# Optimization experiments

Measured on AMD Instinct MI355X. Metric: run time of the kernel, lower is better.

## Reference

```python
import jax, jax.numpy as jnp
import numpy as np

BATCH = 8192
EMBED_DIM = 256
INPUT_DIM = 3 * EMBED_DIM  # 768
NUM_LAYERS = 4
VOCAB_SIZES = [100000, 100000, 1000]
EPS = 1e-5


def setup_inputs() -> dict:
    key = jax.random.key(0)
    ks = jax.random.split(key, 20)
    inp = {}
    inp["x_p"] = jax.random.randint(ks[0], (BATCH,), 0, VOCAB_SIZES[0])
    inp["x_a"] = jax.random.randint(ks[1], (BATCH,), 0, VOCAB_SIZES[1])
    inp["x_c"] = jax.random.randint(ks[2], (BATCH,), 0, VOCAB_SIZES[2])
    inp["y_true"] = jax.random.uniform(ks[3], (BATCH, 1), dtype=jnp.float32)
    # embedding tables (nn.Embedding default init N(0,1))
    inp["E0"] = jax.random.normal(ks[4], (VOCAB_SIZES[0], EMBED_DIM), dtype=jnp.float32)
    inp["E1"] = jax.random.normal(ks[5], (VOCAB_SIZES[1], EMBED_DIM), dtype=jnp.float32)
    inp["E2"] = jax.random.normal(ks[6], (VOCAB_SIZES[2], EMBED_DIM), dtype=jnp.float32)
    lim = 1.0 / np.sqrt(INPUT_DIM)
    inp["Wd"] = jax.random.uniform(ks[7], (NUM_LAYERS, INPUT_DIM, INPUT_DIM), jnp.float32, -lim, lim)
    inp["bd"] = jnp.zeros((NUM_LAYERS, INPUT_DIM), jnp.float32)
    inp["Ws"] = jax.random.uniform(ks[8], (NUM_LAYERS, INPUT_DIM, INPUT_DIM), jnp.float32, -lim, lim)
    inp["bs"] = jnp.zeros((NUM_LAYERS, INPUT_DIM), jnp.float32)
    inp["wfd"] = jax.random.uniform(ks[9], (INPUT_DIM,), jnp.float32, -lim, lim)
    inp["bfd"] = jax.random.uniform(ks[10], (), jnp.float32, -lim, lim)
    inp["wfs"] = jax.random.uniform(ks[11], (INPUT_DIM,), jnp.float32, -lim, lim)
    inp["bfs"] = jax.random.uniform(ks[12], (), jnp.float32, -lim, lim)
    return inp


def _cross_network(x, W, b, net_id, mask_key):
    # per layer: cross = x @ W[l].T + b[l]; mask = bernoulli(sigmoid(layernorm over FULL tensor)); x += cross*mask
    for l in range(NUM_LAYERS):
        cross = jnp.einsum("bd,od->bo", x, W[l]) + b[l]
        m = jnp.mean(cross)
        v = jnp.mean(jnp.square(cross - m))  # F.layer_norm(x, x.size()): normalize over all elements
        ln = (cross - m) * jax.lax.rsqrt(v + EPS)
        p = jax.nn.sigmoid(ln)
        k = jax.random.fold_in(mask_key, net_id * NUM_LAYERS + l)
        mask = jax.random.bernoulli(k, p).astype(x.dtype)
        x = x + cross * mask
    return x


def _bce(p, y):
    return jnp.mean(-(y * jnp.log(p) + (1.0 - y) * jnp.log(1.0 - p)))


def reference(x_p, x_a, x_c, y_true, E0, E1, E2, Wd, bd, Ws, bs, wfd, bfd, wfs, bfs):
    h = EMBED_DIM // 2
    e0, e1, e2 = E0[x_p], E1[x_a], E2[x_c]  # [B, embed_dim] each
    e_a = jnp.concatenate([e0[:, :h], e1[:, :h], e2[:, :h]], axis=-1)
    e_b = jnp.concatenate([e0[:, h:], e1[:, h:], e2[:, h:]], axis=-1)
    x = jnp.concatenate([e_a, e_b], axis=-1)  # [B, 3*embed_dim]

    mask_key = jax.random.key(42)
    x_d = _cross_network(x, Wd, bd, 0, mask_key)
    x_s = _cross_network(x, Ws, bs, 1, mask_key)

    sd_d = jax.nn.sigmoid(x_d @ wfd + bfd)[:, None]  # fc_d(x_d)
    ss_s = jax.nn.sigmoid(x_s @ wfs + bfs)[:, None]  # fc_s(x_s)
    sd_s = jax.nn.sigmoid(x_s @ wfd + bfd)[:, None]  # fc_d(x_s)
    ss_d = jax.nn.sigmoid(x_d @ wfs + bfs)[:, None]  # fc_s(x_d)
    y_pred_d = 0.5 * (sd_d + ss_s)
    y_pred_s = 0.5 * (sd_s + ss_d)

    loss_d = _bce(y_pred_d, y_true)
    loss_s = _bce(y_pred_s, y_true)
    bce_loss = loss_d + loss_s
    weight_d = jnp.maximum(0.0, loss_d - bce_loss)
    weight_s = jnp.maximum(0.0, loss_s - bce_loss)
    tri_loss = bce_loss + weight_d * loss_d + weight_s * loss_s
    return (y_pred_d, tri_loss)
```

## Files before the change

kernel.cpp:

```cpp
#include <hip/hip_runtime.h>
#include <hip/hip_bf16.h>
#include <cstdint>
#include <cstddef>

#define BATCH   8192
#define DIM     768
#define NTOT    6291456
#define NLAYERS 4

typedef _Float16 half8 __attribute__((ext_vector_type(8)));
typedef float    f32x4 __attribute__((ext_vector_type(4)));

#define AS_GLOBAL __attribute__((address_space(1)))
#define AS_LDS    __attribute__((address_space(3)))

__device__ __forceinline__ void async_copy16(const void* g, void* l) {
  __builtin_amdgcn_global_load_lds((AS_GLOBAL const uint32_t*)g,
                                   (AS_LDS uint32_t*)l, 16, 0, 0);
}


__host__ __device__ __forceinline__ uint32_t rotl32(uint32_t v, int d) {
  return (v << d) | (v >> (32 - d));
}

__host__ __device__ __forceinline__ void threefry2x32(
    uint32_t k0, uint32_t k1, uint32_t x0, uint32_t x1,
    uint32_t& o0, uint32_t& o1) {
  uint32_t ks2 = k0 ^ k1 ^ 0x1BD11BDAu;
  x0 += k0; x1 += k1;
#define TF_R(r) { x0 += x1; x1 = rotl32(x1, (r)) ^ x0; }
  TF_R(13) TF_R(15) TF_R(26) TF_R(6)
  x0 += k1; x1 += ks2 + 1u;
  TF_R(17) TF_R(29) TF_R(16) TF_R(24)
  x0 += ks2; x1 += k0 + 2u;
  TF_R(13) TF_R(15) TF_R(26) TF_R(6)
  x0 += k0; x1 += k1 + 3u;
  TF_R(17) TF_R(29) TF_R(16) TF_R(24)
  x0 += k1; x1 += ks2 + 4u;
  TF_R(13) TF_R(15) TF_R(26) TF_R(6)
  x0 += ks2; x1 += k0 + 5u;
#undef TF_R
  o0 = x0; o1 = x1;
}

__device__ __forceinline__ double sigmoid_d(double x) {
  return 1.0 / (1.0 + exp(-x));
}

__device__ __forceinline__ double dexp(double x) {
  x = fmin(fmax(x, -708.0), 708.0);
  const double LOG2E = 1.4426950408889634;
  const double LN2   = 0.6931471805599453;
  double t = x * LOG2E;
  double n = rint(t);
  double g = (t - n) * LN2;
  double r = 2.7557319223985893e-07;
  r = r * g + 2.7557319223985888e-06;
  r = r * g + 2.4801587301587302e-05;
  r = r * g + 1.9841269841269841e-04;
  r = r * g + 1.3888888888888889e-03;
  r = r * g + 8.3333333333333332e-03;
  r = r * g + 4.1666666666666664e-02;
  r = r * g + 1.6666666666666666e-01;
  r = r * g + 0.5;
  r = r * g + 1.0;
  r = r * g + 1.0;
  int ni = (int)n;
  double sc = __longlong_as_double(((long long)(1023 + ni)) << 52);
  return r * sc;
}

__global__ __launch_bounds__(256) void gather_kernel(
    const int* __restrict__ x_p, const int* __restrict__ x_a,
    const int* __restrict__ x_c,
    const float* __restrict__ E0, const float* __restrict__ E1,
    const float* __restrict__ E2,
    _Float16* __restrict__ xdh, _Float16* __restrict__ xdl,
    _Float16* __restrict__ xsh, _Float16* __restrict__ xsl,
    double* __restrict__ stats, double* __restrict__ bce_acc) {
  if (blockIdx.x == 0 && threadIdx.x < 18) {
    if (threadIdx.x < 16) stats[threadIdx.x] = 0.0;
    else bce_acc[threadIdx.x - 16] = 0.0;
  }
  int gid = blockIdx.x * 256 + threadIdx.x;
  int g = gid >> 13;
  int b = gid & 8191;
  int f0 = g * 8;
  int half_ = f0 >= 384;
  int w = f0 - 384 * half_;
  int tbl = w >> 7;
  int c0 = (w & 127) + (half_ << 7);
  int row;
  const float* E;
  if (tbl == 0)      { E = E0; row = x_p[b]; }
  else if (tbl == 1) { E = E1; row = x_a[b]; }
  else               { E = E2; row = x_c[b]; }
  const float* src = &E[(size_t)row * 256 + c0];
  f32x4 v0 = *(const f32x4*)src;
  f32x4 v1 = *(const f32x4*)(src + 4);
  half8 h, l;
#pragma unroll
  for (int i = 0; i < 4; ++i) {
    h[i] = (_Float16)v0[i];
    l[i] = (_Float16)(v0[i] - (float)h[i]);
    h[i + 4] = (_Float16)v1[i];
    l[i + 4] = (_Float16)(v1[i] - (float)h[i + 4]);
  }
  size_t o = (size_t)gid * 8;
  *(half8*)&xdh[o] = h; *(half8*)&xdl[o] = l;
  *(half8*)&xsh[o] = h; *(half8*)&xsl[o] = l;
}

__global__ __launch_bounds__(256) void split_w_kernel(
    const float* __restrict__ Wd, const float* __restrict__ Ws,
    _Float16* __restrict__ Wh, _Float16* __restrict__ Wl) {
  int gid = blockIdx.x * 256 + threadIdx.x;
  int nl = gid / 73728;
  int r3 = gid - nl * 73728;
  int t  = r3 / 3072;
  int r4 = r3 - t * 3072;
  int kk = r4 / 768;
  int row = r4 - kk * 768;
  int k0 = t * 32 + kk * 8;
  const float* src = ((nl < 4) ? Wd : Ws) +
                     ((size_t)(nl & 3) * 768 + row) * 768 + k0;
  f32x4 v0 = *(const f32x4*)src;
  f32x4 v1 = *(const f32x4*)(src + 4);
  half8 h, l;
#pragma unroll
  for (int i = 0; i < 4; ++i) {
    h[i] = (_Float16)v0[i];
    l[i] = (_Float16)(v0[i] - (float)h[i]);
    h[i + 4] = (_Float16)v1[i];
    l[i + 4] = (_Float16)(v1[i] - (float)h[i + 4]);
  }
  size_t o = (size_t)gid * 8;
  *(half8*)&Wh[o] = h;
  *(half8*)&Wl[o] = l;
}

__global__ __launch_bounds__(256, 2) void gemm_mfma_kernel(
    const _Float16* __restrict__ xdh, const _Float16* __restrict__ xdl,
    const _Float16* __restrict__ xsh, const _Float16* __restrict__ xsl,
    const _Float16* __restrict__ Wh, const _Float16* __restrict__ Wl,
    const float* __restrict__ bd, const float* __restrict__ bs,
    float* __restrict__ crd, float* __restrict__ crs,
    double* __restrict__ stats, int layer) {
  const int net = blockIdx.z;
  const float* bias = (net ? bs : bd) + layer * DIM;
  float* C = net ? crs : crd;

  const int tid  = threadIdx.x;
  const int wave = tid >> 6, lane = tid & 63;
  const int quad = lane >> 4, l16 = lane & 15;
  const int m0 = blockIdx.x * 128;
  const int n0 = blockIdx.y * 192;

  __shared__ _Float16 lds[2 * 20480];

  const _Float16* xh = net ? xsh : xdh;
  const _Float16* xl = net ? xsl : xdl;
  const size_t wpanel = ((size_t)net * NLAYERS + layer) * (size_t)(24 * 4 * 768 * 8);
  const _Float16* wh = Wh + wpanel;
  const _Float16* wl = Wl + wpanel;

  const int dslot0 = (wave == 0) ? 0 : (wave == 1) ? 512 : (wave == 2) ? 1280 : 1920;
  const int dslot8 = (wave == 0) ? 1024 : (wave == 1) ? 1152 : (wave == 2) ? 1792 : 2432;

  const _Float16* gp[10];
  int gstr[10];
  int dbyte[10];
#pragma unroll
  for (int j = 0; j < 10; ++j) {
    int sb = (j < 8) ? dslot0 + j * 64 : dslot8 + (j - 8) * 64;
    dbyte[j] = sb * 16;
    int s = sb + lane;
    if (s < 1024) {
      int s2 = s & 511;
      int kk = s2 >> 7, r = s2 & 127;
      gp[j] = ((s < 512) ? xh : xl) + (size_t)(kk * 8192 + m0 + r) * 8;
      gstr[j] = 4 * 8192 * 8;
    } else {
      int s2 = s - 1024;
      int s3 = (s2 >= 768) ? s2 - 768 : s2;
      int kk = (s3 * 683) >> 17;
      int r  = s3 - kk * 192;
      gp[j] = ((s2 >= 768) ? wl : wh) + (size_t)(kk * 768 + n0 + r) * 8;
      gstr[j] = 4 * 768 * 8;
    }
  }

  const int wm = (wave >> 1) * 64;
  const int wn = (wave & 1) * 96;

  f32x4 acc[4][6];
#pragma unroll
  for (int i = 0; i < 4; ++i)
#pragma unroll
    for (int j = 0; j < 6; ++j) acc[i][j] = (f32x4){0.f, 0.f, 0.f, 0.f};

#pragma unroll
  for (int j = 0; j < 10; ++j)
    async_copy16(gp[j], (char*)lds + dbyte[j]);
  __syncthreads();

  int cur = 0;
  for (int t = 0; t < 24; ++t) {
    if (t < 23) {
#pragma unroll
      for (int j = 0; j < 10; ++j)
        async_copy16(gp[j] + (t + 1) * gstr[j],
                     (char*)lds + (cur ^ 1) * 40960 + dbyte[j]);
    }
    const _Float16* L = lds + cur * 20480;
    half8 ah[4], al[4];
#pragma unroll
    for (int mt = 0; mt < 4; ++mt) {
      int sl = quad * 128 + wm + mt * 16 + l16;
      ah[mt] = *(const half8*)&L[sl * 8];
      al[mt] = *(const half8*)&L[sl * 8 + 4096];
    }
    __builtin_amdgcn_s_setprio(1);
#pragma unroll
    for (int nt = 0; nt < 6; ++nt) {
      int sl = 1024 + quad * 192 + wn + nt * 16 + l16;
      half8 bh = *(const half8*)&L[sl * 8];
      half8 bl = *(const half8*)&L[sl * 8 + 6144];
#pragma unroll
      for (int mt = 0; mt < 4; ++mt) {
        f32x4 a = acc[mt][nt];
        a = __builtin_amdgcn_mfma_f32_16x16x32_f16(ah[mt], bh, a, 0, 0, 0);
        a = __builtin_amdgcn_mfma_f32_16x16x32_f16(al[mt], bh, a, 0, 0, 0);
        a = __builtin_amdgcn_mfma_f32_16x16x32_f16(ah[mt], bl, a, 0, 0, 0);
        acc[mt][nt] = a;
      }
    }
    __builtin_amdgcn_s_setprio(0);
    __syncthreads();
    cur ^= 1;
  }

  float biasv[6];
#pragma unroll
  for (int nt = 0; nt < 6; ++nt) biasv[nt] = bias[n0 + wn + nt * 16 + l16];

  double S = 0.0, Q = 0.0;
#pragma unroll
  for (int mt = 0; mt < 4; ++mt) {
#pragma unroll
    for (int nt = 0; nt < 6; ++nt) {
      int n = n0 + wn + nt * 16 + l16;
      size_t gbase = (size_t)(n >> 4) * 131072;
#pragma unroll
      for (int r = 0; r < 4; ++r) {
        int m = m0 + wm + mt * 16 + quad * 4 + r;
        float v = acc[mt][nt][r] + biasv[nt];
        C[gbase + m * 16 + l16] = v;
        S += (double)v;
        Q += (double)v * (double)v;
      }
    }
  }
#pragma unroll
  for (int off = 32; off > 0; off >>= 1) {
    S += __shfl_down(S, off);
    Q += __shfl_down(Q, off);
  }
  double* red = (double*)lds;
  if (lane == 0) { red[wave * 2] = S; red[wave * 2 + 1] = Q; }
  __syncthreads();
  if (tid == 0) {
    double s2 = 0.0, q2 = 0.0;
#pragma unroll
    for (int wv = 0; wv < 4; ++wv) { s2 += red[wv * 2]; q2 += red[wv * 2 + 1]; }
    double* st = stats + ((size_t)layer * 2 + net) * 2;
    atomicAdd(&st[0], s2);
    atomicAdd(&st[1], q2);
  }
}

__global__ __launch_bounds__(256) void mask_update_kernel(
    _Float16* __restrict__ xdh, _Float16* __restrict__ xdl,
    _Float16* __restrict__ xsh, _Float16* __restrict__ xsl,
    const float* __restrict__ crd, const float* __restrict__ crs,
    const double* __restrict__ stats, int layer,
    uint32_t kd0, uint32_t kd1, uint32_t ks0, uint32_t ks1) {
  const int net = blockIdx.y;
  _Float16* xh = net ? xsh : xdh;
  _Float16* xl = net ? xsl : xdl;
  const float* cr = net ? crs : crd;
  const uint32_t k0 = net ? ks0 : kd0;
  const uint32_t k1 = net ? ks1 : kd1;

  const double invN = 1.0 / (double)NTOT;
  const double* st = stats + ((size_t)layer * 2 + net) * 2;
  double meand = st[0] * invN;
  double vard  = st[1] * invN - meand * meand;
  float m  = (float)meand;
  float sv = (float)vard + 1e-5f;
  float rs = (float)(1.0 / sqrt((double)sv));

  int cg = blockIdx.x * 256 + threadIdx.x;
  int g16 = cg >> 13;
  int b   = cg & 8191;
  int f0  = g16 * 16;

  f32x4 c4[4];
#pragma unroll
  for (int i = 0; i < 4; ++i) c4[i] = *(const f32x4*)&cr[(size_t)cg * 16 + i * 4];

  size_t xg0 = ((size_t)g16 * 2) * 8192 + b;
  half8 h0 = *(const half8*)&xh[xg0 * 8];
  half8 l0 = *(const half8*)&xl[xg0 * 8];
  half8 h1 = *(const half8*)&xh[(xg0 + 8192) * 8];
  half8 l1 = *(const half8*)&xl[(xg0 + 8192) * 8];
  half8 ho0, lo0, ho1, lo1;

#pragma unroll
  for (int i = 0; i < 16; ++i) {
    float c  = c4[i >> 2][i & 3];
    float ln = (c - m) * rs;
    uint32_t o0, o1;
    threefry2x32(k0, k1, 0u, (uint32_t)(b * 768 + f0 + i), o0, o1);
    uint32_t bits = o0 ^ o1;
    float u = __uint_as_float(0x3F800000u | (bits >> 9)) - 1.0f;
    double e  = dexp(-(double)ln);
    double ue = (double)u;
    float xv = (i < 8) ? ((float)h0[i & 7] + (float)l0[i & 7])
                       : ((float)h1[i & 7] + (float)l1[i & 7]);
    if (ue + ue * e < 1.0) xv += c;
    _Float16 hh = (_Float16)xv;
    _Float16 ll = (_Float16)(xv - (float)hh);
    if (i < 8) { ho0[i & 7] = hh; lo0[i & 7] = ll; }
    else       { ho1[i & 7] = hh; lo1[i & 7] = ll; }
  }
  *(half8*)&xh[xg0 * 8] = ho0;
  *(half8*)&xl[xg0 * 8] = lo0;
  *(half8*)&xh[(xg0 + 8192) * 8] = ho1;
  *(half8*)&xl[(xg0 + 8192) * 8] = lo1;
}

__global__ __launch_bounds__(256) void head_kernel(
    const _Float16* __restrict__ xdh, const _Float16* __restrict__ xdl,
    const _Float16* __restrict__ xsh, const _Float16* __restrict__ xsl,
    const float* __restrict__ wfd, const float* __restrict__ wfs,
    const float* __restrict__ bfd_p, const float* __restrict__ bfs_p,
    const float* __restrict__ y_true,
    float* __restrict__ out, double* __restrict__ bce_acc) {
  int b = blockIdx.x * 256 + threadIdx.x;
  float dd = 0.f, dsw = 0.f, sd = 0.f, ssw = 0.f;
  for (int g = 0; g < 96; ++g) {
    size_t o = ((size_t)g * 8192 + b) * 8;
    half8 hd = *(const half8*)&xdh[o];
    half8 ld = *(const half8*)&xdl[o];
    half8 hs = *(const half8*)&xsh[o];
    half8 ls = *(const half8*)&xsl[o];
#pragma unroll
    for (int i = 0; i < 8; ++i) {
      float vd = (float)hd[i] + (float)ld[i];
      float vs = (float)hs[i] + (float)ls[i];
      float wd = wfd[g * 8 + i], ws = wfs[g * 8 + i];
      dd  = fmaf(vd, wd, dd);
      dsw = fmaf(vd, ws, dsw);
      sd  = fmaf(vs, wd, sd);
      ssw = fmaf(vs, ws, ssw);
    }
  }
  float bfd = *bfd_p, bfs = *bfs_p;
  double sdd = sigmoid_d((double)(dd + bfd));
  double ssd = sigmoid_d((double)(dsw + bfs));
  double sds = sigmoid_d((double)(sd + bfd));
  double sss = sigmoid_d((double)(ssw + bfs));
  double ypd = 0.5 * (sdd + sss);
  double yps = 0.5 * (sds + ssd);
  out[b] = (float)ypd;
  double y = (double)y_true[b];
  double bce_d = -(y * log(ypd) + (1.0 - y) * log(1.0 - ypd));
  double bce_s = -(y * log(yps) + (1.0 - y) * log(1.0 - yps));
#pragma unroll
  for (int off = 32; off > 0; off >>= 1) {
    bce_d += __shfl_down(bce_d, off);
    bce_s += __shfl_down(bce_s, off);
  }
  __shared__ double redd[4], reds[4];
  int wave = threadIdx.x >> 6, lane = threadIdx.x & 63;
  if (lane == 0) { redd[wave] = bce_d; reds[wave] = bce_s; }
  __syncthreads();
  if (threadIdx.x == 0) {
    atomicAdd(&bce_acc[0], redd[0] + redd[1] + redd[2] + redd[3]);
    atomicAdd(&bce_acc[1], reds[0] + reds[1] + reds[2] + reds[3]);
  }
}

__global__ void loss_kernel(const double* __restrict__ bce_acc,
                            float* __restrict__ out_tri) {
  if (threadIdx.x == 0) {
    double loss_d = bce_acc[0] / (double)BATCH;
    double loss_s = bce_acc[1] / (double)BATCH;
    double bce = loss_d + loss_s;
    double wd = fmax(0.0, loss_d - bce);
    double ws = fmax(0.0, loss_s - bce);
    out_tri[0] = (float)(bce + wd * loss_d + ws * loss_s);
  }
}

extern "C" void kernel_launch(void* const* d_in, const int* in_sizes, int n_in,
                              void* d_out, int out_size, void* d_ws, size_t ws_size,
                              hipStream_t stream) {
  const int* x_p = (const int*)d_in[0];
  const int* x_a = (const int*)d_in[1];
  const int* x_c = (const int*)d_in[2];
  const float* y_true = (const float*)d_in[3];
  const float* E0 = (const float*)d_in[4];
  const float* E1 = (const float*)d_in[5];
  const float* E2 = (const float*)d_in[6];
  const float* Wd = (const float*)d_in[7];
  const float* bd = (const float*)d_in[8];
  const float* Ws = (const float*)d_in[9];
  const float* bs = (const float*)d_in[10];
  const float* wfd = (const float*)d_in[11];
  const float* bfd = (const float*)d_in[12];
  const float* wfs = (const float*)d_in[13];
  const float* bfs = (const float*)d_in[14];
  float* out = (float*)d_out;

  char* p = (char*)d_ws;
  float* crd = (float*)p;                 p += (size_t)NTOT * 4;
  float* crs = (float*)p;                 p += (size_t)NTOT * 4;
  double* stats   = (double*)p;           p += (size_t)16 * 8;
  double* bce_acc = (double*)p;           p += (size_t)2 * 8;
  _Float16* xdh = (_Float16*)p;           p += (size_t)NTOT * 2;
  _Float16* xdl = (_Float16*)p;           p += (size_t)NTOT * 2;
  _Float16* xsh = (_Float16*)p;           p += (size_t)NTOT * 2;
  _Float16* xsl = (_Float16*)p;           p += (size_t)NTOT * 2;
  _Float16* Wh  = (_Float16*)p;           p += (size_t)2 * NLAYERS * DIM * DIM * 2;
  _Float16* Wl  = (_Float16*)p;           p += (size_t)2 * NLAYERS * DIM * DIM * 2;

  gather_kernel<<<NTOT / 8 / 256, 256, 0, stream>>>(
      x_p, x_a, x_c, E0, E1, E2, xdh, xdl, xsh, xsl, stats, bce_acc);
  split_w_kernel<<<2 * NLAYERS * DIM * DIM / 8 / 256, 256, 0, stream>>>(
      Wd, Ws, Wh, Wl);

  for (int l = 0; l < NLAYERS; ++l) {
    gemm_mfma_kernel<<<dim3(64, 4, 2), 256, 0, stream>>>(
        xdh, xdl, xsh, xsl, Wh, Wl, bd, bs, crd, crs, stats, l);
    uint32_t kd0, kd1, ks0, ks1;
    threefry2x32(0u, 42u, 0u, (uint32_t)l, kd0, kd1);
    threefry2x32(0u, 42u, 0u, (uint32_t)(4 + l), ks0, ks1);
    mask_update_kernel<<<dim3(NTOT / 16 / 256, 2), 256, 0, stream>>>(
        xdh, xdl, xsh, xsl, crd, crs, stats, l, kd0, kd1, ks0, ks1);
  }

  head_kernel<<<BATCH / 256, 256, 0, stream>>>(
      xdh, xdl, xsh, xsl, wfd, wfs, bfd, bfs, y_true, out, bce_acc);
  loss_kernel<<<1, 64, 0, stream>>>(bce_acc, out + BATCH);
}
```

Before: 667.9 us.

## Use 8-wave GEMM blocks, load low-part A directly, split head reduction

The GEMM block grows from 4 to 8 waves, each computing a 64x48 sub-tile, with smaller accumulator arrays to allow higher occupancy. The low half of the activation split is no longer staged through LDS; each wave reads it straight from global memory, which shrinks the LDS footprint. The MFMA calls are regrouped into three passes per tile. The head kernel now splits the 768-wide dot product across four waves per 64 rows and combines the partials in shared memory, giving it more blocks. The direct global loads of the low part sit outside the async prefetch and can add latency inside the main loop.

```diff
diff --git a/kernel.cpp b/kernel.cpp
--- a/kernel.cpp
+++ b/kernel.cpp
@@ -140,7 +140,7 @@
   *(half8*)&Wl[o] = l;
 }
 
-__global__ __launch_bounds__(256, 2) void gemm_mfma_kernel(
+__global__ __launch_bounds__(512, 4) void gemm_mfma_kernel(
     const _Float16* __restrict__ xdh, const _Float16* __restrict__ xdl,
     const _Float16* __restrict__ xsh, const _Float16* __restrict__ xsl,
     const _Float16* __restrict__ Wh, const _Float16* __restrict__ Wl,
@@ -157,7 +157,7 @@
   const int m0 = blockIdx.x * 128;
   const int n0 = blockIdx.y * 192;
 
-  __shared__ _Float16 lds[2 * 20480];
+  __shared__ _Float16 lds[2 * 16384];
 
   const _Float16* xh = net ? xsh : xdh;
   const _Float16* xl = net ? xsl : xdl;
@@ -165,24 +165,20 @@
   const _Float16* wh = Wh + wpanel;
   const _Float16* wl = Wl + wpanel;
 
-  const int dslot0 = (wave == 0) ? 0 : (wave == 1) ? 512 : (wave == 2) ? 1280 : 1920;
-  const int dslot8 = (wave == 0) ? 1024 : (wave == 1) ? 1152 : (wave == 2) ? 1792 : 2432;
-
-  const _Float16* gp[10];
-  int gstr[10];
-  int dbyte[10];
-#pragma unroll
-  for (int j = 0; j < 10; ++j) {
-    int sb = (j < 8) ? dslot0 + j * 64 : dslot8 + (j - 8) * 64;
+  const _Float16* gp[4];
+  int gstr[4];
+  int dbyte[4];
+#pragma unroll
+  for (int j = 0; j < 4; ++j) {
+    int sb = wave * 256 + j * 64;
     dbyte[j] = sb * 16;
     int s = sb + lane;
-    if (s < 1024) {
-      int s2 = s & 511;
-      int kk = s2 >> 7, r = s2 & 127;
-      gp[j] = ((s < 512) ? xh : xl) + (size_t)(kk * 8192 + m0 + r) * 8;
+    if (s < 512) {
+      int kk = s >> 7, r = s & 127;
+      gp[j] = xh + (size_t)(kk * 8192 + m0 + r) * 8;
       gstr[j] = 4 * 8192 * 8;
     } else {
-      int s2 = s - 1024;
+      int s2 = s - 512;
       int s3 = (s2 >= 768) ? s2 - 768 : s2;
       int kk = (s3 * 683) >> 17;
       int r  = s3 - kk * 192;
@@ -191,17 +187,19 @@
     }
   }
 
-  const int wm = (wave >> 1) * 64;
-  const int wn = (wave & 1) * 96;
-
-  f32x4 acc[4][6];
+  const int wm = (wave >> 2) * 64;
+  const int wn = (wave & 3) * 48;
+
+  const _Float16* alb = xl + (size_t)(quad * 8192 + m0 + wm + l16) * 8;
+
+  f32x4 acc[4][3];
 #pragma unroll
   for (int i = 0; i < 4; ++i)
 #pragma unroll
-    for (int j = 0; j < 6; ++j) acc[i][j] = (f32x4){0.f, 0.f, 0.f, 0.f};
-
-#pragma unroll
-  for (int j = 0; j < 10; ++j)
+    for (int j = 0; j < 3; ++j) acc[i][j] = (f32x4){0.f, 0.f, 0.f, 0.f};
+
+#pragma unroll
+  for (int j = 0; j < 4; ++j)
     async_copy16(gp[j], (char*)lds + dbyte[j]);
   __syncthreads();
 
@@ -209,47 +207,57 @@
   for (int t = 0; t < 24; ++t) {
     if (t < 23) {
 #pragma unroll
-      for (int j = 0; j < 10; ++j)
+      for (int j = 0; j < 4; ++j)
         async_copy16(gp[j] + (t + 1) * gstr[j],
-                     (char*)lds + (cur ^ 1) * 40960 + dbyte[j]);
-    }
-    const _Float16* L = lds + cur * 20480;
-    half8 ah[4], al[4];
-#pragma unroll
-    for (int mt = 0; mt < 4; ++mt) {
-      int sl = quad * 128 + wm + mt * 16 + l16;
-      ah[mt] = *(const half8*)&L[sl * 8];
-      al[mt] = *(const half8*)&L[sl * 8 + 4096];
+                     (char*)lds + (cur ^ 1) * 32768 + dbyte[j]);
+    }
+    const _Float16* alt = alb + t * 262144;
+    half8 al[4];
+#pragma unroll
+    for (int mt = 0; mt < 4; ++mt)
+      al[mt] = *(const half8*)(alt + mt * 128);
+
+    const _Float16* L = lds + cur * 16384;
+    half8 ah[4], bh[3], bl[3];
+#pragma unroll
+    for (int mt = 0; mt < 4; ++mt)
+      ah[mt] = *(const half8*)&L[(quad * 128 + wm + mt * 16 + l16) * 8];
+#pragma unroll
+    for (int nt = 0; nt < 3; ++nt) {
+      int ss = 512 + quad * 192 + wn + nt * 16 + l16;
+      bh[nt] = *(const half8*)&L[ss * 8];
+      bl[nt] = *(const half8*)&L[ss * 8 + 6144];
     }
     __builtin_amdgcn_s_setprio(1);
 #pragma unroll
-    for (int nt = 0; nt < 6; ++nt) {
-      int sl = 1024 + quad * 192 + wn + nt * 16 + l16;
-      half8 bh = *(const half8*)&L[sl * 8];
-      half8 bl = *(const half8*)&L[sl * 8 + 6144];
-#pragma unroll
-      for (int mt = 0; mt < 4; ++mt) {
-        f32x4 a = acc[mt][nt];
-        a = __builtin_amdgcn_mfma_f32_16x16x32_f16(ah[mt], bh, a, 0, 0, 0);
-        a = __builtin_amdgcn_mfma_f32_16x16x32_f16(al[mt], bh, a, 0, 0, 0);
-        a = __builtin_amdgcn_mfma_f32_16x16x32_f16(ah[mt], bl, a, 0, 0, 0);
-        acc[mt][nt] = a;
-      }
-    }
+    for (int nt = 0; nt < 3; ++nt)
+#pragma unroll
+      for (int mt = 0; mt < 4; ++mt)
+        acc[mt][nt] = __builtin_amdgcn_mfma_f32_16x16x32_f16(ah[mt], bh[nt], acc[mt][nt], 0, 0, 0);
+#pragma unroll
+    for (int nt = 0; nt < 3; ++nt)
+#pragma unroll
+      for (int mt = 0; mt < 4; ++mt)
+        acc[mt][nt] = __builtin_amdgcn_mfma_f32_16x16x32_f16(ah[mt], bl[nt], acc[mt][nt], 0, 0, 0);
+#pragma unroll
+    for (int nt = 0; nt < 3; ++nt)
+#pragma unroll
+      for (int mt = 0; mt < 4; ++mt)
+        acc[mt][nt] = __builtin_amdgcn_mfma_f32_16x16x32_f16(al[mt], bh[nt], acc[mt][nt], 0, 0, 0);
     __builtin_amdgcn_s_setprio(0);
     __syncthreads();
     cur ^= 1;
   }
 
-  float biasv[6];
-#pragma unroll
-  for (int nt = 0; nt < 6; ++nt) biasv[nt] = bias[n0 + wn + nt * 16 + l16];
+  float biasv[3];
+#pragma unroll
+  for (int nt = 0; nt < 3; ++nt) biasv[nt] = bias[n0 + wn + nt * 16 + l16];
 
   double S = 0.0, Q = 0.0;
 #pragma unroll
   for (int mt = 0; mt < 4; ++mt) {
 #pragma unroll
-    for (int nt = 0; nt < 6; ++nt) {
+    for (int nt = 0; nt < 3; ++nt) {
       int n = n0 + wn + nt * 16 + l16;
       size_t gbase = (size_t)(n >> 4) * 131072;
 #pragma unroll
@@ -273,7 +281,7 @@
   if (tid == 0) {
     double s2 = 0.0, q2 = 0.0;
 #pragma unroll
-    for (int wv = 0; wv < 4; ++wv) { s2 += red[wv * 2]; q2 += red[wv * 2 + 1]; }
+    for (int wv = 0; wv < 8; ++wv) { s2 += red[wv * 2]; q2 += red[wv * 2 + 1]; }
     double* st = stats + ((size_t)layer * 2 + net) * 2;
     atomicAdd(&st[0], s2);
     atomicAdd(&st[1], q2);
@@ -348,10 +356,14 @@
     const float* __restrict__ bfd_p, const float* __restrict__ bfs_p,
     const float* __restrict__ y_true,
     float* __restrict__ out, double* __restrict__ bce_acc) {
-  int b = blockIdx.x * 256 + threadIdx.x;
+  const int tq = threadIdx.x >> 6;
+  const int tb = threadIdx.x & 63;
+  const int row = blockIdx.x * 64 + tb;
+
   float dd = 0.f, dsw = 0.f, sd = 0.f, ssw = 0.f;
-  for (int g = 0; g < 96; ++g) {
-    size_t o = ((size_t)g * 8192 + b) * 8;
+  const int g0 = tq * 24;
+  for (int g = g0; g < g0 + 24; ++g) {
+    size_t o = ((size_t)g * 8192 + row) * 8;
     half8 hd = *(const half8*)&xdh[o];
     half8 ld = *(const half8*)&xdl[o];
     half8 hs = *(const half8*)&xsh[o];
@@ -367,29 +379,36 @@
       ssw = fmaf(vs, ws, ssw);
     }
   }
-  float bfd = *bfd_p, bfs = *bfs_p;
-  double sdd = sigmoid_d((double)(dd + bfd));
-  double ssd = sigmoid_d((double)(dsw + bfs));
-  double sds = sigmoid_d((double)(sd + bfd));
-  double sss = sigmoid_d((double)(ssw + bfs));
-  double ypd = 0.5 * (sdd + sss);
-  double yps = 0.5 * (sds + ssd);
-  out[b] = (float)ypd;
-  double y = (double)y_true[b];
-  double bce_d = -(y * log(ypd) + (1.0 - y) * log(1.0 - ypd));
-  double bce_s = -(y * log(yps) + (1.0 - y) * log(1.0 - yps));
-#pragma unroll
-  for (int off = 32; off > 0; off >>= 1) {
-    bce_d += __shfl_down(bce_d, off);
-    bce_s += __shfl_down(bce_s, off);
-  }
-  __shared__ double redd[4], reds[4];
-  int wave = threadIdx.x >> 6, lane = threadIdx.x & 63;
-  if (lane == 0) { redd[wave] = bce_d; reds[wave] = bce_s; }
+  __shared__ float part[4][64][4];
+  part[tq][tb][0] = dd;  part[tq][tb][1] = dsw;
+  part[tq][tb][2] = sd;  part[tq][tb][3] = ssw;
   __syncthreads();
-  if (threadIdx.x == 0) {
-    atomicAdd(&bce_acc[0], redd[0] + redd[1] + redd[2] + redd[3]);
-    atomicAdd(&bce_acc[1], reds[0] + reds[1] + reds[2] + reds[3]);
+
+  if (threadIdx.x < 64) {
+    float DD  = part[0][tb][0] + part[1][tb][0] + part[2][tb][0] + part[3][tb][0];
+    float DSW = part[0][tb][1] + part[1][tb][1] + part[2][tb][1] + part[3][tb][1];
+    float SD  = part[0][tb][2] + part[1][tb][2] + part[2][tb][2] + part[3][tb][2];
+    float SSW = part[0][tb][3] + part[1][tb][3] + part[2][tb][3] + part[3][tb][3];
+    float bfd = *bfd_p, bfs = *bfs_p;
+    double sdd = sigmoid_d((double)(DD + bfd));
+    double ssd = sigmoid_d((double)(DSW + bfs));
+    double sds = sigmoid_d((double)(SD + bfd));
+    double sss = sigmoid_d((double)(SSW + bfs));
+    double ypd = 0.5 * (sdd + sss);
+    double yps = 0.5 * (sds + ssd);
+    out[row] = (float)ypd;
+    double y = (double)y_true[row];
+    double bce_d = -(y * log(ypd) + (1.0 - y) * log(1.0 - ypd));
+    double bce_s = -(y * log(yps) + (1.0 - y) * log(1.0 - yps));
+#pragma unroll
+    for (int off = 32; off > 0; off >>= 1) {
+      bce_d += __shfl_down(bce_d, off);
+      bce_s += __shfl_down(bce_s, off);
+    }
+    if (tb == 0) {
+      atomicAdd(&bce_acc[0], bce_d);
+      atomicAdd(&bce_acc[1], bce_s);
+    }
   }
 }
 
@@ -443,7 +462,7 @@
       Wd, Ws, Wh, Wl);
 
   for (int l = 0; l < NLAYERS; ++l) {
-    gemm_mfma_kernel<<<dim3(64, 4, 2), 256, 0, stream>>>(
+    gemm_mfma_kernel<<<dim3(64, 4, 2), 512, 0, stream>>>(
         xdh, xdl, xsh, xsl, Wh, Wl, bd, bs, crd, crs, stats, l);
     uint32_t kd0, kd1, ks0, ks1;
     threefry2x32(0u, 42u, 0u, (uint32_t)l, kd0, kd1);
@@ -452,7 +471,7 @@
         xdh, xdl, xsh, xsl, crd, crs, stats, l, kd0, kd1, ks0, ks1);
   }
 
-  head_kernel<<<BATCH / 256, 256, 0, stream>>>(
+  head_kernel<<<BATCH / 64, 256, 0, stream>>>(
       xdh, xdl, xsh, xsl, wfd, wfs, bfd, bfs, y_true, out, bce_acc);
   loss_kernel<<<1, 64, 0, stream>>>(bce_acc, out + BATCH);
 }
```

Measured after the change: 667.9 us. Within noise of the previous version (+0.0%).
